# Performance work log

Hardware: AMD Instinct MI355X
Metric: run time of the kernel (lower is better)

## Reference

```python
import jax, jax.numpy as jnp
import numpy as np

N, L, D = 512, 40, 128      # batch, peptide length, embedding dim
O, K, MHC = 256, 9, 34      # out_channels, kernel_size, mhc_len
STRIDE = 1


def setup_inputs() -> dict:
    key = jax.random.key(0)
    k1, k2, k3 = jax.random.split(key, 3)
    peptide_x = jax.random.normal(k1, (N, L, D), dtype=jnp.float32)
    mhc_x = jax.random.normal(k2, (N, MHC, D), dtype=jnp.float32)
    weight = jax.random.normal(k3, (O, K, MHC), dtype=jnp.float32) * 0.02  # truncated_normal std=0.02 approx
    bias = jnp.zeros((O,), dtype=jnp.float32)
    return {"peptide_x": peptide_x, "mhc_x": mhc_x, "weight": weight, "bias": bias}


def reference(peptide_x, mhc_x, weight, bias):
    # Per-sample dynamic kernel generation: [n, O, d, K]
    kernel = jax.nn.relu(jnp.einsum('nld,okl->nodk', mhc_x, weight))
    k = weight.shape[1]
    T = (peptide_x.shape[1] - k) // STRIDE + 1  # conv1d output length
    # Sliding windows of the peptide: [n, T, K, d]
    idx = jnp.arange(T)[:, None] * STRIDE + jnp.arange(k)[None, :]
    win = peptide_x[:, idx, :]
    # Grouped (groups=batch) conv1d as a batched contraction: [n, O, T]
    out = jnp.einsum('ntkd,nodk->not', win, kernel) + bias[None, :, None]
    return out
```

## Files before the change

kernel.cpp:

```cpp
#include <hip/hip_runtime.h>
#include <hip/hip_bf16.h>

typedef unsigned short u16;
typedef unsigned int u32;
typedef __bf16 bf16x8 __attribute__((ext_vector_type(8)));
typedef float f32x4 __attribute__((ext_vector_type(4)));
typedef unsigned int u32x4 __attribute__((ext_vector_type(4)));
typedef unsigned int u32x2 __attribute__((ext_vector_type(2)));

#define NN 512
#define LL 40
#define DD 128
#define OO 256
#define KK 9
#define MHCL 34
#define TT 32
#define PSTR 136
#define MSTR 72
#define KDSTR 72
#define LPAD 64
#define WPADL 64

#define PEPT_U16 (LL * PSTR)
#define KS_U16   (32 * KDSTR)

__device__ __forceinline__ u16 f2bf(float x) {
    unsigned int u = __builtin_bit_cast(unsigned int, x);
    u = (u + 0x7FFFu + ((u >> 16) & 1u)) >> 16;
    return (u16)u;
}
__device__ __forceinline__ u32 pk2(float a, float b) {
    __hip_bfloat162 h = __float22bfloat162_rn(make_float2(a, b));
    u32 r;
    __builtin_memcpy(&r, &h, 4);
    return r;
}
__device__ __forceinline__ bf16x8 lds_read8(const u16* p) {
    u32x4 r;
    __builtin_memcpy(&r, __builtin_assume_aligned(p, 16), 16);
    return __builtin_bit_cast(bf16x8, r);
}
__device__ __forceinline__ f32x4 mfma16(bf16x8 a, bf16x8 b, f32x4 c) {
    return __builtin_amdgcn_mfma_f32_16x16x32_bf16(a, b, c, 0, 0, 0);
}

__global__ void w_convert(const float* __restrict__ wgt, u32* __restrict__ wp) {
    int i = blockIdx.x * 256 + threadIdx.x;
    if (i >= OO * KK * (WPADL / 2)) return;
    int o = i / (KK * (WPADL / 2));
    int r = i - o * (KK * (WPADL / 2));
    int k = r >> 5;
    int lp = (r & 31) << 1;
    const float* src = wgt + ((size_t)o * KK + k) * MHCL;
    float a = (lp     < MHCL) ? src[lp]     : 0.f;
    float b = (lp + 1 < MHCL) ? src[lp + 1] : 0.f;
    wp[i] = pk2(a, b);
}

template<bool PRE>
__global__ __launch_bounds__(256, 2)
void iconv_kernel(const float* __restrict__ pept,
                  const float* __restrict__ mhc,
                  const float* __restrict__ wgt,
                  const u16* __restrict__ wp,
                  const float* __restrict__ bias,
                  float* __restrict__ out)
{
    __shared__ __align__(16) u16 s_mem[PEPT_U16 + 4 * KS_U16];

    const int tid  = threadIdx.x;
    const int wave = tid >> 6;
    const int pair = wave >> 1;
    const int dh   = wave & 1;
    const int lane = tid & 63;
    const int quad = lane >> 4;
    const int l16  = lane & 15;

    const int n  = blockIdx.x >> 1;
    const int oh = blockIdx.x & 1;

    u16* const s_pept = s_mem;
    u16* const ks     = s_mem + PEPT_U16 + wave * KS_U16;

    auto loadW = [&](int o_base, int k, bf16x8 wF[2][2]) {
        if (PRE) {
            #pragma unroll
            for (int mt = 0; mt < 2; ++mt) {
                const u16* wr = wp + ((size_t)(o_base + mt * 16 + l16) * KK + k) * WPADL;
                u32x4 r0, r1;
                __builtin_memcpy(&r0, __builtin_assume_aligned(wr + quad * 8, 16), 16);
                __builtin_memcpy(&r1, __builtin_assume_aligned(wr + 32 + quad * 8, 16), 16);
                wF[mt][0] = __builtin_bit_cast(bf16x8, r0);
                wF[mt][1] = __builtin_bit_cast(bf16x8, r1);
            }
        } else {
            #pragma unroll
            for (int mt = 0; mt < 2; ++mt) {
                const float* wrow = wgt + ((size_t)(o_base + mt * 16 + l16) * KK + k) * MHCL;
                float w8[8];
                __builtin_memcpy(w8, __builtin_assume_aligned(wrow + quad * 8, 8), 32);
                u16 h0[8];
                #pragma unroll
                for (int j = 0; j < 8; ++j) h0[j] = f2bf(w8[j]);
                __builtin_memcpy(&wF[mt][0], h0, 16);
                u16 h1[8] = {0,0,0,0,0,0,0,0};
                if (quad == 0) { h1[0] = f2bf(wrow[32]); h1[1] = f2bf(wrow[33]); }
                __builtin_memcpy(&wF[mt][1], h1, 16);
            }
        }
    };

    bf16x8 wB[2][2];
    loadW((oh * 4 + pair * 2) * 32, 0, wB);

    {
        const float* mg = mhc + (size_t)n * MHCL * DD;
        #pragma unroll 1
        for (int i = tid; i < DD * (LPAD / 8); i += 256) {
            int g = i >> 7, d = i & 127;
            u32x4 hh;
            #pragma unroll
            for (int jj = 0; jj < 4; ++jj) {
                int l = g * 8 + jj * 2;
                float a = (l     < MHCL) ? mg[(size_t)l * DD + d]       : 0.f;
                float b = (l + 1 < MHCL) ? mg[(size_t)(l + 1) * DD + d] : 0.f;
                hh[jj] = pk2(a, b);
            }
            __builtin_memcpy(__builtin_assume_aligned(&s_mem[d * MSTR + g * 8], 16), &hh, 16);
        }
    }
    __syncthreads();

    bf16x8 mA[4][2];
    #pragma unroll
    for (int di = 0; di < 4; ++di) {
        const int d = dh * 64 + di * 16 + l16;
        mA[di][0] = lds_read8(&s_mem[d * MSTR + quad * 8]);
        mA[di][1] = lds_read8(&s_mem[d * MSTR + 32 + quad * 8]);
    }
    __syncthreads();

    {
        const float* pg = pept + (size_t)n * LL * DD;
        #pragma unroll 1
        for (int i = tid; i < (LL * DD) / 4; i += 256) {
            int row = i >> 5, c4 = (i & 31) << 2;
            f32x4 v;
            __builtin_memcpy(&v, __builtin_assume_aligned(pg + row * DD + c4, 16), 16);
            u32x2 h = { pk2(v[0], v[1]), pk2(v[2], v[3]) };
            __builtin_memcpy(__builtin_assume_aligned(&s_pept[row * PSTR + c4], 8), &h, 8);
        }
    }
    __syncthreads();

    #pragma unroll 1
    for (int oci = 0; oci < 2; ++oci) {
        const int obase = (oh * 4 + pair * 2 + oci) * 32;
        f32x4 acc00 = {0.f,0.f,0.f,0.f}, acc01 = acc00, acc10 = acc00, acc11 = acc00;

        #pragma unroll 3
        for (int k = 0; k < KK; ++k) {
            #pragma unroll
            for (int di = 0; di < 4; ++di) {
                f32x4 c0 = {0.f,0.f,0.f,0.f}, c1 = c0;
                c0 = mfma16(mA[di][0], wB[0][0], c0);
                c0 = mfma16(mA[di][1], wB[0][1], c0);
                c1 = mfma16(mA[di][0], wB[1][0], c1);
                c1 = mfma16(mA[di][1], wB[1][1], c1);
                u32x2 p0 = { pk2(fmaxf(c0[0], 0.f), fmaxf(c0[1], 0.f)),
                             pk2(fmaxf(c0[2], 0.f), fmaxf(c0[3], 0.f)) };
                u32x2 p1 = { pk2(fmaxf(c1[0], 0.f), fmaxf(c1[1], 0.f)),
                             pk2(fmaxf(c1[2], 0.f), fmaxf(c1[3], 0.f)) };
                __builtin_memcpy(__builtin_assume_aligned(&ks[l16 * KDSTR + di * 16 + quad * 4], 8), &p0, 8);
                __builtin_memcpy(__builtin_assume_aligned(&ks[(16 + l16) * KDSTR + di * 16 + quad * 4], 8), &p1, 8);
            }
            if (k < KK - 1)    loadW(obase, k + 1, wB);
            else if (oci == 0) loadW(obase + 32, 0, wB);
            #pragma unroll
            for (int ds = 0; ds < 2; ++ds) {
                bf16x8 kb0 = lds_read8(&ks[l16 * KDSTR + ds * 32 + quad * 8]);
                bf16x8 kb1 = lds_read8(&ks[(16 + l16) * KDSTR + ds * 32 + quad * 8]);
                bf16x8 ap0 = lds_read8(&s_pept[(k + l16) * PSTR + dh * 64 + ds * 32 + quad * 8]);
                bf16x8 ap1 = lds_read8(&s_pept[(k + 16 + l16) * PSTR + dh * 64 + ds * 32 + quad * 8]);
                acc00 = mfma16(ap0, kb0, acc00);
                acc01 = mfma16(ap0, kb1, acc01);
                acc10 = mfma16(ap1, kb0, acc10);
                acc11 = mfma16(ap1, kb1, acc11);
            }
        }

        if (dh == 1) {
            float* ox = (float*)ks;
            const int fb = lane * 16;
            __builtin_memcpy(__builtin_assume_aligned(&ox[fb +  0], 16), &acc00, 16);
            __builtin_memcpy(__builtin_assume_aligned(&ox[fb +  4], 16), &acc01, 16);
            __builtin_memcpy(__builtin_assume_aligned(&ox[fb +  8], 16), &acc10, 16);
            __builtin_memcpy(__builtin_assume_aligned(&ox[fb + 12], 16), &acc11, 16);
        }
        __syncthreads();
        if (dh == 0) {
            const float* px = (const float*)(s_mem + PEPT_U16 + (wave + 1) * KS_U16);
            const int fb = lane * 16;
            f32x4 q00, q01, q10, q11;
            __builtin_memcpy(&q00, __builtin_assume_aligned(&px[fb +  0], 16), 16);
            __builtin_memcpy(&q01, __builtin_assume_aligned(&px[fb +  4], 16), 16);
            __builtin_memcpy(&q10, __builtin_assume_aligned(&px[fb +  8], 16), 16);
            __builtin_memcpy(&q11, __builtin_assume_aligned(&px[fb + 12], 16), 16);
            const float bv0 = bias[obase + l16];
            const float bv1 = bias[obase + 16 + l16];
            f32x4 r00 = acc00 + q00 + bv0;
            f32x4 r01 = acc01 + q01 + bv1;
            f32x4 r10 = acc10 + q10 + bv0;
            f32x4 r11 = acc11 + q11 + bv1;
            float* ob = out + ((size_t)n * OO + obase) * TT;
            __builtin_memcpy(__builtin_assume_aligned(ob + (size_t)l16 * TT + quad * 4, 16), &r00, 16);
            __builtin_memcpy(__builtin_assume_aligned(ob + (size_t)(16 + l16) * TT + quad * 4, 16), &r01, 16);
            __builtin_memcpy(__builtin_assume_aligned(ob + (size_t)l16 * TT + 16 + quad * 4, 16), &r10, 16);
            __builtin_memcpy(__builtin_assume_aligned(ob + (size_t)(16 + l16) * TT + 16 + quad * 4, 16), &r11, 16);
        }
        __syncthreads();
    }
}

extern "C" void kernel_launch(void* const* d_in, const int* in_sizes, int n_in,
                              void* d_out, int out_size, void* d_ws, size_t ws_size,
                              hipStream_t stream) {
    const float* pept = (const float*)d_in[0];
    const float* mhc  = (const float*)d_in[1];
    const float* wgt  = (const float*)d_in[2];
    const float* bias = (const float*)d_in[3];
    float* out = (float*)d_out;

    const size_t w_bytes = (size_t)OO * KK * WPADL * sizeof(u16);
    if (ws_size >= w_bytes) {
        w_convert<<<dim3((OO * KK * (WPADL / 2) + 255) / 256), dim3(256), 0, stream>>>(wgt, (u32*)d_ws);
        iconv_kernel<true><<<dim3(NN * 2), dim3(256), 0, stream>>>(pept, mhc, wgt, (const u16*)d_ws, bias, out);
    } else {
        iconv_kernel<false><<<dim3(NN * 2), dim3(256), 0, stream>>>(pept, mhc, wgt, nullptr, bias, out);
    }
}
```

Baseline: 117.5 us.

## Double-buffer per-wave kernel tile and load MHC fragments directly from global

Gives each wave two LDS kernel buffers so it can build the next k's dynamic kernel tile (stage-1 MFMA, ReLU, bf16 pack) while the current k's conv MFMAs run, and prefetches weights two steps ahead. The MHC A-fragments are now loaded straight from global into registers, dropping the LDS staging pass and two block barriers. Fully unrolling the k loop and holding two weight sets plus preloaded fragments raises register pressure, and LDS use per block grows, which may affect occupancy. The strided global reads for MHC are also less coalesced.

```diff
diff --git a/kernel.cpp b/kernel.cpp
--- a/kernel.cpp
+++ b/kernel.cpp
@@ -16,9 +16,7 @@
 #define MHCL 34
 #define TT 32
 #define PSTR 136
-#define MSTR 72
 #define KDSTR 72
-#define LPAD 64
 #define WPADL 64
 
 #define PEPT_U16 (LL * PSTR)
@@ -66,7 +64,7 @@
                   const float* __restrict__ bias,
                   float* __restrict__ out)
 {
-    __shared__ __align__(16) u16 s_mem[PEPT_U16 + 4 * KS_U16];
+    __shared__ __align__(16) u16 s_mem[PEPT_U16 + 8 * KS_U16];
 
     const int tid  = threadIdx.x;
     const int wave = tid >> 6;
@@ -80,7 +78,8 @@
     const int oh = blockIdx.x & 1;
 
     u16* const s_pept = s_mem;
-    u16* const ks     = s_mem + PEPT_U16 + wave * KS_U16;
+    u16* const ks0    = s_mem + PEPT_U16 + wave * (2 * KS_U16);
+    u16* const ks1    = ks0 + KS_U16;
 
     auto loadW = [&](int o_base, int k, bf16x8 wF[2][2]) {
         if (PRE) {
@@ -113,32 +112,25 @@
     bf16x8 wB[2][2];
     loadW((oh * 4 + pair * 2) * 32, 0, wB);
 
+    bf16x8 mA[4][2];
     {
         const float* mg = mhc + (size_t)n * MHCL * DD;
-        #pragma unroll 1
-        for (int i = tid; i < DD * (LPAD / 8); i += 256) {
-            int g = i >> 7, d = i & 127;
-            u32x4 hh;
-            #pragma unroll
-            for (int jj = 0; jj < 4; ++jj) {
-                int l = g * 8 + jj * 2;
-                float a = (l     < MHCL) ? mg[(size_t)l * DD + d]       : 0.f;
-                float b = (l + 1 < MHCL) ? mg[(size_t)(l + 1) * DD + d] : 0.f;
-                hh[jj] = pk2(a, b);
-            }
-            __builtin_memcpy(__builtin_assume_aligned(&s_mem[d * MSTR + g * 8], 16), &hh, 16);
-        }
-    }
-    __syncthreads();
-
-    bf16x8 mA[4][2];
-    #pragma unroll
-    for (int di = 0; di < 4; ++di) {
-        const int d = dh * 64 + di * 16 + l16;
-        mA[di][0] = lds_read8(&s_mem[d * MSTR + quad * 8]);
-        mA[di][1] = lds_read8(&s_mem[d * MSTR + 32 + quad * 8]);
-    }
-    __syncthreads();
+        #pragma unroll
+        for (int di = 0; di < 4; ++di) {
+            const int d = dh * 64 + di * 16 + l16;
+            u16 h0[8];
+            #pragma unroll
+            for (int j = 0; j < 8; ++j)
+                h0[j] = f2bf(mg[(size_t)(quad * 8 + j) * DD + d]);
+            __builtin_memcpy(&mA[di][0], h0, 16);
+            u16 h1[8] = {0,0,0,0,0,0,0,0};
+            if (quad == 0) {
+                h1[0] = f2bf(mg[(size_t)32 * DD + d]);
+                h1[1] = f2bf(mg[(size_t)33 * DD + d]);
+            }
+            __builtin_memcpy(&mA[di][1], h1, 16);
+        }
+    }
 
     {
         const float* pg = pept + (size_t)n * LL * DD;
@@ -153,44 +145,57 @@
     }
     __syncthreads();
 
+    auto stage1 = [&](const bf16x8 wF[2][2], u16* kbw) {
+        #pragma unroll
+        for (int di = 0; di < 4; ++di) {
+            f32x4 c0 = {0.f,0.f,0.f,0.f}, c1 = c0;
+            c0 = mfma16(mA[di][0], wF[0][0], c0);
+            c0 = mfma16(mA[di][1], wF[0][1], c0);
+            c1 = mfma16(mA[di][0], wF[1][0], c1);
+            c1 = mfma16(mA[di][1], wF[1][1], c1);
+            u32x2 p0 = { pk2(fmaxf(c0[0], 0.f), fmaxf(c0[1], 0.f)),
+                         pk2(fmaxf(c0[2], 0.f), fmaxf(c0[3], 0.f)) };
+            u32x2 p1 = { pk2(fmaxf(c1[0], 0.f), fmaxf(c1[1], 0.f)),
+                         pk2(fmaxf(c1[2], 0.f), fmaxf(c1[3], 0.f)) };
+            __builtin_memcpy(__builtin_assume_aligned(&kbw[l16 * KDSTR + di * 16 + quad * 4], 8), &p0, 8);
+            __builtin_memcpy(__builtin_assume_aligned(&kbw[(16 + l16) * KDSTR + di * 16 + quad * 4], 8), &p1, 8);
+        }
+    };
+
     #pragma unroll 1
     for (int oci = 0; oci < 2; ++oci) {
         const int obase = (oh * 4 + pair * 2 + oci) * 32;
         f32x4 acc00 = {0.f,0.f,0.f,0.f}, acc01 = acc00, acc10 = acc00, acc11 = acc00;
 
-        #pragma unroll 3
+        stage1(wB, ks0);
+        loadW(obase, 1, wB);
+
+        #pragma unroll
         for (int k = 0; k < KK; ++k) {
-            #pragma unroll
-            for (int di = 0; di < 4; ++di) {
-                f32x4 c0 = {0.f,0.f,0.f,0.f}, c1 = c0;
-                c0 = mfma16(mA[di][0], wB[0][0], c0);
-                c0 = mfma16(mA[di][1], wB[0][1], c0);
-                c1 = mfma16(mA[di][0], wB[1][0], c1);
-                c1 = mfma16(mA[di][1], wB[1][1], c1);
-                u32x2 p0 = { pk2(fmaxf(c0[0], 0.f), fmaxf(c0[1], 0.f)),
-                             pk2(fmaxf(c0[2], 0.f), fmaxf(c0[3], 0.f)) };
-                u32x2 p1 = { pk2(fmaxf(c1[0], 0.f), fmaxf(c1[1], 0.f)),
-                             pk2(fmaxf(c1[2], 0.f), fmaxf(c1[3], 0.f)) };
-                __builtin_memcpy(__builtin_assume_aligned(&ks[l16 * KDSTR + di * 16 + quad * 4], 8), &p0, 8);
-                __builtin_memcpy(__builtin_assume_aligned(&ks[(16 + l16) * KDSTR + di * 16 + quad * 4], 8), &p1, 8);
-            }
-            if (k < KK - 1)    loadW(obase, k + 1, wB);
-            else if (oci == 0) loadW(obase + 32, 0, wB);
+            u16* const kr = (k & 1) ? ks1 : ks0;
+            u16* const kw = (k & 1) ? ks0 : ks1;
+            bf16x8 kbv[2][2], apv[2][2];
             #pragma unroll
             for (int ds = 0; ds < 2; ++ds) {
-                bf16x8 kb0 = lds_read8(&ks[l16 * KDSTR + ds * 32 + quad * 8]);
-                bf16x8 kb1 = lds_read8(&ks[(16 + l16) * KDSTR + ds * 32 + quad * 8]);
-                bf16x8 ap0 = lds_read8(&s_pept[(k + l16) * PSTR + dh * 64 + ds * 32 + quad * 8]);
-                bf16x8 ap1 = lds_read8(&s_pept[(k + 16 + l16) * PSTR + dh * 64 + ds * 32 + quad * 8]);
-                acc00 = mfma16(ap0, kb0, acc00);
-                acc01 = mfma16(ap0, kb1, acc01);
-                acc10 = mfma16(ap1, kb0, acc10);
-                acc11 = mfma16(ap1, kb1, acc11);
+                kbv[ds][0] = lds_read8(&kr[l16 * KDSTR + ds * 32 + quad * 8]);
+                kbv[ds][1] = lds_read8(&kr[(16 + l16) * KDSTR + ds * 32 + quad * 8]);
+                apv[ds][0] = lds_read8(&s_pept[(k + l16) * PSTR + dh * 64 + ds * 32 + quad * 8]);
+                apv[ds][1] = lds_read8(&s_pept[(k + 16 + l16) * PSTR + dh * 64 + ds * 32 + quad * 8]);
+            }
+            if (k < KK - 1) stage1(wB, kw);
+            if (k < KK - 2) loadW(obase, k + 2, wB);
+            else if (k == KK - 2 && oci == 0) loadW(obase + 32, 0, wB);
+            #pragma unroll
+            for (int ds = 0; ds < 2; ++ds) {
+                acc00 = mfma16(apv[ds][0], kbv[ds][0], acc00);
+                acc01 = mfma16(apv[ds][0], kbv[ds][1], acc01);
+                acc10 = mfma16(apv[ds][1], kbv[ds][0], acc10);
+                acc11 = mfma16(apv[ds][1], kbv[ds][1], acc11);
             }
         }
 
         if (dh == 1) {
-            float* ox = (float*)ks;
+            float* ox = (float*)ks0;
             const int fb = lane * 16;
             __builtin_memcpy(__builtin_assume_aligned(&ox[fb +  0], 16), &acc00, 16);
             __builtin_memcpy(__builtin_assume_aligned(&ox[fb +  4], 16), &acc01, 16);
@@ -199,7 +204,7 @@
         }
         __syncthreads();
         if (dh == 0) {
-            const float* px = (const float*)(s_mem + PEPT_U16 + (wave + 1) * KS_U16);
+            const float* px = (const float*)(s_mem + PEPT_U16 + (wave + 1) * (2 * KS_U16));
             const int fb = lane * 16;
             f32x4 q00, q01, q10, q11;
             __builtin_memcpy(&q00, __builtin_assume_aligned(&px[fb +  0], 16), 16);
```

Result: no change. 117.8 us (+0.2%).

## Split each sample across four blocks and load MHC fragments directly from global

Applied to the files above, without the earlier changes.

The grid doubles from 2 to 4 blocks per sample, so each wave pair now handles one 32-channel output chunk instead of looping over two. The MHC operand fragments are read straight from global memory into registers and converted to bf16, which removes the LDS staging pass and two block barriers. This gives more parallelism and a shorter per-block critical path. In exchange, the peptide tile is loaded and converted twice as often, and the per-lane strided global reads of MHC are poorly coalesced.

```diff
diff --git a/kernel.cpp b/kernel.cpp
--- a/kernel.cpp
+++ b/kernel.cpp
@@ -16,9 +16,7 @@
 #define MHCL 34
 #define TT 32
 #define PSTR 136
-#define MSTR 72
 #define KDSTR 72
-#define LPAD 64
 #define WPADL 64
 
 #define PEPT_U16 (LL * PSTR)
@@ -76,8 +74,9 @@
     const int quad = lane >> 4;
     const int l16  = lane & 15;
 
-    const int n  = blockIdx.x >> 1;
-    const int oh = blockIdx.x & 1;
+    const int n  = blockIdx.x >> 2;
+    const int oq = blockIdx.x & 3;
+    const int obase = (oq * 2 + pair) * 32;
 
     u16* const s_pept = s_mem;
     u16* const ks     = s_mem + PEPT_U16 + wave * KS_U16;
@@ -111,34 +110,27 @@
     };
 
     bf16x8 wB[2][2];
-    loadW((oh * 4 + pair * 2) * 32, 0, wB);
-
+    loadW(obase, 0, wB);
+
+    bf16x8 mA[4][2];
     {
         const float* mg = mhc + (size_t)n * MHCL * DD;
-        #pragma unroll 1
-        for (int i = tid; i < DD * (LPAD / 8); i += 256) {
-            int g = i >> 7, d = i & 127;
-            u32x4 hh;
+        #pragma unroll
+        for (int di = 0; di < 4; ++di) {
+            const int d = dh * 64 + di * 16 + l16;
+            u16 h0[8];
             #pragma unroll
-            for (int jj = 0; jj < 4; ++jj) {
-                int l = g * 8 + jj * 2;
-                float a = (l     < MHCL) ? mg[(size_t)l * DD + d]       : 0.f;
-                float b = (l + 1 < MHCL) ? mg[(size_t)(l + 1) * DD + d] : 0.f;
-                hh[jj] = pk2(a, b);
+            for (int j = 0; j < 8; ++j)
+                h0[j] = f2bf(mg[(size_t)(quad * 8 + j) * DD + d]);
+            __builtin_memcpy(&mA[di][0], h0, 16);
+            u16 h1[8] = {0,0,0,0,0,0,0,0};
+            if (quad == 0) {
+                h1[0] = f2bf(mg[(size_t)32 * DD + d]);
+                h1[1] = f2bf(mg[(size_t)33 * DD + d]);
             }
-            __builtin_memcpy(__builtin_assume_aligned(&s_mem[d * MSTR + g * 8], 16), &hh, 16);
-        }
-    }
-    __syncthreads();
-
-    bf16x8 mA[4][2];
-    #pragma unroll
-    for (int di = 0; di < 4; ++di) {
-        const int d = dh * 64 + di * 16 + l16;
-        mA[di][0] = lds_read8(&s_mem[d * MSTR + quad * 8]);
-        mA[di][1] = lds_read8(&s_mem[d * MSTR + 32 + quad * 8]);
-    }
-    __syncthreads();
+            __builtin_memcpy(&mA[di][1], h1, 16);
+        }
+    }
 
     {
         const float* pg = pept + (size_t)n * LL * DD;
@@ -153,72 +145,66 @@
     }
     __syncthreads();
 
-    #pragma unroll 1
-    for (int oci = 0; oci < 2; ++oci) {
-        const int obase = (oh * 4 + pair * 2 + oci) * 32;
-        f32x4 acc00 = {0.f,0.f,0.f,0.f}, acc01 = acc00, acc10 = acc00, acc11 = acc00;
-
-        #pragma unroll 3
-        for (int k = 0; k < KK; ++k) {
-            #pragma unroll
-            for (int di = 0; di < 4; ++di) {
-                f32x4 c0 = {0.f,0.f,0.f,0.f}, c1 = c0;
-                c0 = mfma16(mA[di][0], wB[0][0], c0);
-                c0 = mfma16(mA[di][1], wB[0][1], c0);
-                c1 = mfma16(mA[di][0], wB[1][0], c1);
-                c1 = mfma16(mA[di][1], wB[1][1], c1);
-                u32x2 p0 = { pk2(fmaxf(c0[0], 0.f), fmaxf(c0[1], 0.f)),
-                             pk2(fmaxf(c0[2], 0.f), fmaxf(c0[3], 0.f)) };
-                u32x2 p1 = { pk2(fmaxf(c1[0], 0.f), fmaxf(c1[1], 0.f)),
-                             pk2(fmaxf(c1[2], 0.f), fmaxf(c1[3], 0.f)) };
-                __builtin_memcpy(__builtin_assume_aligned(&ks[l16 * KDSTR + di * 16 + quad * 4], 8), &p0, 8);
-                __builtin_memcpy(__builtin_assume_aligned(&ks[(16 + l16) * KDSTR + di * 16 + quad * 4], 8), &p1, 8);
-            }
-            if (k < KK - 1)    loadW(obase, k + 1, wB);
-            else if (oci == 0) loadW(obase + 32, 0, wB);
-            #pragma unroll
-            for (int ds = 0; ds < 2; ++ds) {
-                bf16x8 kb0 = lds_read8(&ks[l16 * KDSTR + ds * 32 + quad * 8]);
-                bf16x8 kb1 = lds_read8(&ks[(16 + l16) * KDSTR + ds * 32 + quad * 8]);
-                bf16x8 ap0 = lds_read8(&s_pept[(k + l16) * PSTR + dh * 64 + ds * 32 + quad * 8]);
-                bf16x8 ap1 = lds_read8(&s_pept[(k + 16 + l16) * PSTR + dh * 64 + ds * 32 + quad * 8]);
-                acc00 = mfma16(ap0, kb0, acc00);
-                acc01 = mfma16(ap0, kb1, acc01);
-                acc10 = mfma16(ap1, kb0, acc10);
-                acc11 = mfma16(ap1, kb1, acc11);
-            }
-        }
-
-        if (dh == 1) {
-            float* ox = (float*)ks;
-            const int fb = lane * 16;
-            __builtin_memcpy(__builtin_assume_aligned(&ox[fb +  0], 16), &acc00, 16);
-            __builtin_memcpy(__builtin_assume_aligned(&ox[fb +  4], 16), &acc01, 16);
-            __builtin_memcpy(__builtin_assume_aligned(&ox[fb +  8], 16), &acc10, 16);
-            __builtin_memcpy(__builtin_assume_aligned(&ox[fb + 12], 16), &acc11, 16);
-        }
-        __syncthreads();
-        if (dh == 0) {
-            const float* px = (const float*)(s_mem + PEPT_U16 + (wave + 1) * KS_U16);
-            const int fb = lane * 16;
-            f32x4 q00, q01, q10, q11;
-            __builtin_memcpy(&q00, __builtin_assume_aligned(&px[fb +  0], 16), 16);
-            __builtin_memcpy(&q01, __builtin_assume_aligned(&px[fb +  4], 16), 16);
-            __builtin_memcpy(&q10, __builtin_assume_aligned(&px[fb +  8], 16), 16);
-            __builtin_memcpy(&q11, __builtin_assume_aligned(&px[fb + 12], 16), 16);
-            const float bv0 = bias[obase + l16];
-            const float bv1 = bias[obase + 16 + l16];
-            f32x4 r00 = acc00 + q00 + bv0;
-            f32x4 r01 = acc01 + q01 + bv1;
-            f32x4 r10 = acc10 + q10 + bv0;
-            f32x4 r11 = acc11 + q11 + bv1;
-            float* ob = out + ((size_t)n * OO + obase) * TT;
-            __builtin_memcpy(__builtin_assume_aligned(ob + (size_t)l16 * TT + quad * 4, 16), &r00, 16);
-            __builtin_memcpy(__builtin_assume_aligned(ob + (size_t)(16 + l16) * TT + quad * 4, 16), &r01, 16);
-            __builtin_memcpy(__builtin_assume_aligned(ob + (size_t)l16 * TT + 16 + quad * 4, 16), &r10, 16);
-            __builtin_memcpy(__builtin_assume_aligned(ob + (size_t)(16 + l16) * TT + 16 + quad * 4, 16), &r11, 16);
-        }
-        __syncthreads();
+    f32x4 acc00 = {0.f,0.f,0.f,0.f}, acc01 = acc00, acc10 = acc00, acc11 = acc00;
+
+    #pragma unroll 3
+    for (int k = 0; k < KK; ++k) {
+        #pragma unroll
+        for (int di = 0; di < 4; ++di) {
+            f32x4 c0 = {0.f,0.f,0.f,0.f}, c1 = c0;
+            c0 = mfma16(mA[di][0], wB[0][0], c0);
+            c0 = mfma16(mA[di][1], wB[0][1], c0);
+            c1 = mfma16(mA[di][0], wB[1][0], c1);
+            c1 = mfma16(mA[di][1], wB[1][1], c1);
+            u32x2 p0 = { pk2(fmaxf(c0[0], 0.f), fmaxf(c0[1], 0.f)),
+                         pk2(fmaxf(c0[2], 0.f), fmaxf(c0[3], 0.f)) };
+            u32x2 p1 = { pk2(fmaxf(c1[0], 0.f), fmaxf(c1[1], 0.f)),
+                         pk2(fmaxf(c1[2], 0.f), fmaxf(c1[3], 0.f)) };
+            __builtin_memcpy(__builtin_assume_aligned(&ks[l16 * KDSTR + di * 16 + quad * 4], 8), &p0, 8);
+            __builtin_memcpy(__builtin_assume_aligned(&ks[(16 + l16) * KDSTR + di * 16 + quad * 4], 8), &p1, 8);
+        }
+        if (k < KK - 1) loadW(obase, k + 1, wB);
+        #pragma unroll
+        for (int ds = 0; ds < 2; ++ds) {
+            bf16x8 kb0 = lds_read8(&ks[l16 * KDSTR + ds * 32 + quad * 8]);
+            bf16x8 kb1 = lds_read8(&ks[(16 + l16) * KDSTR + ds * 32 + quad * 8]);
+            bf16x8 ap0 = lds_read8(&s_pept[(k + l16) * PSTR + dh * 64 + ds * 32 + quad * 8]);
+            bf16x8 ap1 = lds_read8(&s_pept[(k + 16 + l16) * PSTR + dh * 64 + ds * 32 + quad * 8]);
+            acc00 = mfma16(ap0, kb0, acc00);
+            acc01 = mfma16(ap0, kb1, acc01);
+            acc10 = mfma16(ap1, kb0, acc10);
+            acc11 = mfma16(ap1, kb1, acc11);
+        }
+    }
+
+    if (dh == 1) {
+        float* ox = (float*)ks;
+        const int fb = lane * 16;
+        __builtin_memcpy(__builtin_assume_aligned(&ox[fb +  0], 16), &acc00, 16);
+        __builtin_memcpy(__builtin_assume_aligned(&ox[fb +  4], 16), &acc01, 16);
+        __builtin_memcpy(__builtin_assume_aligned(&ox[fb +  8], 16), &acc10, 16);
+        __builtin_memcpy(__builtin_assume_aligned(&ox[fb + 12], 16), &acc11, 16);
+    }
+    __syncthreads();
+    if (dh == 0) {
+        const float* px = (const float*)(s_mem + PEPT_U16 + (wave + 1) * KS_U16);
+        const int fb = lane * 16;
+        f32x4 q00, q01, q10, q11;
+        __builtin_memcpy(&q00, __builtin_assume_aligned(&px[fb +  0], 16), 16);
+        __builtin_memcpy(&q01, __builtin_assume_aligned(&px[fb +  4], 16), 16);
+        __builtin_memcpy(&q10, __builtin_assume_aligned(&px[fb +  8], 16), 16);
+        __builtin_memcpy(&q11, __builtin_assume_aligned(&px[fb + 12], 16), 16);
+        const float bv0 = bias[obase + l16];
+        const float bv1 = bias[obase + 16 + l16];
+        f32x4 r00 = acc00 + q00 + bv0;
+        f32x4 r01 = acc01 + q01 + bv1;
+        f32x4 r10 = acc10 + q10 + bv0;
+        f32x4 r11 = acc11 + q11 + bv1;
+        float* ob = out + ((size_t)n * OO + obase) * TT;
+        __builtin_memcpy(__builtin_assume_aligned(ob + (size_t)l16 * TT + quad * 4, 16), &r00, 16);
+        __builtin_memcpy(__builtin_assume_aligned(ob + (size_t)(16 + l16) * TT + quad * 4, 16), &r01, 16);
+        __builtin_memcpy(__builtin_assume_aligned(ob + (size_t)l16 * TT + 16 + quad * 4, 16), &r10, 16);
+        __builtin_memcpy(__builtin_assume_aligned(ob + (size_t)(16 + l16) * TT + 16 + quad * 4, 16), &r11, 16);
     }
 }
 
@@ -234,8 +220,8 @@
     const size_t w_bytes = (size_t)OO * KK * WPADL * sizeof(u16);
     if (ws_size >= w_bytes) {
         w_convert<<<dim3((OO * KK * (WPADL / 2) + 255) / 256), dim3(256), 0, stream>>>(wgt, (u32*)d_ws);
-        iconv_kernel<true><<<dim3(NN * 2), dim3(256), 0, stream>>>(pept, mhc, wgt, (const u16*)d_ws, bias, out);
+        iconv_kernel<true><<<dim3(NN * 4), dim3(256), 0, stream>>>(pept, mhc, wgt, (const u16*)d_ws, bias, out);
     } else {
-        iconv_kernel<false><<<dim3(NN * 2), dim3(256), 0, stream>>>(pept, mhc, wgt, nullptr, bias, out);
-    }
-}
+        iconv_kernel<false><<<dim3(NN * 4), dim3(256), 0, stream>>>(pept, mhc, wgt, nullptr, bias, out);
+    }
+}
```

Result: no change. 116.6 us (-0.8%).
